# Performance work log

Hardware: AMD Instinct MI355X
Metric: run time of the kernel (lower is better)

Reference implementation:

```python
import jax, jax.numpy as jnp
import numpy as np

N = 100000      # nodes
E_RAND = 1500000
IN_DIM = 128
OUT_DIM = 128
H = 8
D = OUT_DIM // H  # 16 per-head dim
EPS = 1e-5


def _bn(x, gamma, beta):
    # BatchNorm1d, training mode: biased batch statistics over the node dim
    mu = jnp.mean(x, axis=0)
    var = jnp.mean((x - mu) ** 2, axis=0)
    return (x - mu) * jax.lax.rsqrt(var + EPS) * gamma + beta


def setup_inputs() -> dict:
    key = jax.random.key(0)
    ks = jax.random.split(key, 12)
    h = jax.random.normal(ks[0], (N, IN_DIM), dtype=jnp.float32)
    # edge list: random edges + self-loops so every dst has in-degree >= 1
    src_r = jax.random.randint(ks[1], (E_RAND,), 0, N, dtype=jnp.int32)
    dst_r = jax.random.randint(ks[2], (E_RAND,), 0, N, dtype=jnp.int32)
    loops = jnp.arange(N, dtype=jnp.int32)
    src = jnp.concatenate([loops, src_r])
    dst = jnp.concatenate([loops, dst_r])
    s = 1.0 / np.sqrt(IN_DIM)
    Wq = jax.random.normal(ks[3], (IN_DIM, OUT_DIM), dtype=jnp.float32) * s
    Wk = jax.random.normal(ks[4], (IN_DIM, OUT_DIM), dtype=jnp.float32) * s
    Wv = jax.random.normal(ks[5], (IN_DIM, OUT_DIM), dtype=jnp.float32) * s
    Wo = jax.random.normal(ks[6], (OUT_DIM, OUT_DIM), dtype=jnp.float32) * s
    bo = jnp.zeros((OUT_DIM,), dtype=jnp.float32)
    gamma1 = jnp.ones((OUT_DIM,), dtype=jnp.float32)
    beta1 = jnp.zeros((OUT_DIM,), dtype=jnp.float32)
    Wf1 = jax.random.normal(ks[7], (OUT_DIM, 2 * OUT_DIM), dtype=jnp.float32) * s
    bf1 = jnp.zeros((2 * OUT_DIM,), dtype=jnp.float32)
    Wf2 = jax.random.normal(ks[8], (2 * OUT_DIM, OUT_DIM), dtype=jnp.float32) * (1.0 / np.sqrt(2 * OUT_DIM))
    bf2 = jnp.zeros((OUT_DIM,), dtype=jnp.float32)
    gamma2 = jnp.ones((OUT_DIM,), dtype=jnp.float32)
    beta2 = jnp.zeros((OUT_DIM,), dtype=jnp.float32)
    return {"h": h, "Wq": Wq, "Wk": Wk, "Wv": Wv, "Wo": Wo, "bo": bo,
            "gamma1": gamma1, "beta1": beta1, "Wf1": Wf1, "bf1": bf1,
            "Wf2": Wf2, "bf2": bf2, "gamma2": gamma2, "beta2": beta2,
            "src": src, "dst": dst}


def reference(h, Wq, Wk, Wv, Wo, bo, gamma1, beta1, Wf1, bf1, Wf2, bf2,
              gamma2, beta2, src, dst):
    n = h.shape[0]
    Q = (h @ Wq).reshape(n, H, D)
    K = (h @ Wk).reshape(n, H, D)
    V = (h @ Wv).reshape(n, H, D)
    # per-edge score: (K[src] * Q[dst]).sum(-1), scaled exp with clamp
    score = jnp.sum(K[src] * Q[dst], axis=-1) / np.sqrt(D)   # [E, H]
    score = jnp.exp(jnp.clip(score, -5.0, 5.0))
    # weighted aggregation to dst nodes
    wV = jax.ops.segment_sum(V[src] * score[:, :, None], dst, num_segments=n)  # [N,H,D]
    z = jax.ops.segment_sum(score, dst, num_segments=n)                         # [N,H]
    attn = (wV / z[:, :, None]).reshape(n, OUT_DIM)
    # output projection + residual + batchnorm
    x = h + (attn @ Wo + bo)
    x = _bn(x, gamma1, beta1)
    # FFN + residual + batchnorm
    y = jax.nn.relu(x @ Wf1 + bf1) @ Wf2 + bf2
    x = _bn(x + y, gamma2, beta2)
    return x
```

## Files before the change

### kernel.cpp

```cpp
#include <hip/hip_runtime.h>

#define EPS 1e-5f
#define VSCALE 20.0f

typedef __attribute__((ext_vector_type(8))) short sh8;
typedef __attribute__((ext_vector_type(4))) float f4;
typedef __attribute__((ext_vector_type(2))) _Float16 h2f;

static __device__ __forceinline__ unsigned short f2b(float f) {
    union { float f; unsigned u; } v; v.f = f;
    unsigned r = v.u + 0x7FFF + ((v.u >> 16) & 1);
    return (unsigned short)(r >> 16);
}
static __device__ __forceinline__ float b2f(unsigned short b) {
    union { unsigned u; float f; } v; v.u = ((unsigned)b) << 16; return v.f;
}
static __device__ __forceinline__ unsigned pk2(float a, float b) {
    return (unsigned)f2b(a) | ((unsigned)f2b(b) << 16);
}
static __device__ __forceinline__ h2f u2h(unsigned u) {
    union { unsigned u; h2f h; } c; c.u = u; return c.h;
}
static __device__ __forceinline__ float dot2h(h2f a, h2f b, float c) {
#if __has_builtin(__builtin_amdgcn_fdot2)
    return __builtin_amdgcn_fdot2(a, b, c, false);
#else
    return (float)a.x * (float)b.x + (float)a.y * (float)b.y + c;
#endif
}

static __device__ __forceinline__ void barrier_raw() {
    __builtin_amdgcn_sched_barrier(0);
    asm volatile("s_waitcnt lgkmcnt(0)" ::: "memory");
    __builtin_amdgcn_s_barrier();
    __builtin_amdgcn_sched_barrier(0);
}

__global__ __launch_bounds__(256) void prep_all_k(
    const float* __restrict__ Wq, const float* __restrict__ Wk,
    const float* __restrict__ Wv, const float* __restrict__ Wo,
    const float* __restrict__ Wf1, const float* __restrict__ Wf2,
    unsigned short* __restrict__ Wt)
{
    int i = blockIdx.x * 256 + threadIdx.x;
    if (i < 65536) {
        int s = i >> 14;
        const float* W = (s == 0) ? Wq : (s == 1) ? Wk : (s == 2) ? Wv : Wo;
        int l = i & 16383, k = l >> 7, n = l & 127;
        Wt[(i & ~16383) + n * 128 + k] = f2b(W[l]);
    } else if (i < 98304) {
        int l = i - 65536, k = l >> 8, n = l & 255;
        Wt[65536 + n * 128 + k] = f2b(Wf1[l]);
    } else {
        int l = i - 98304, k = l >> 7, n = l & 127;
        Wt[98304 + n * 256 + k] = f2b(Wf2[l]);
    }
}

__global__ __launch_bounds__(256) void qkv_k(
    const float* __restrict__ h, const unsigned short* __restrict__ Wt,
    _Float16* __restrict__ Qh, _Float16* __restrict__ Kh,
    unsigned char* __restrict__ V8u, int M)
{
    __shared__ __align__(16) unsigned short As[128 * 136];
    __shared__ __align__(16) unsigned short Ws[128 * 72];
    const int tid = threadIdx.x;
    const int wave = tid >> 6, lane = tid & 63;
    const int q = lane >> 4, lm = lane & 15;
    const int rowBase = blockIdx.x * 128;
    const int r0 = (wave & 1) * 64, c0 = (wave >> 1) * 64;

#pragma unroll
    for (int j = 0; j < 16; ++j) {
        int idx = tid + j * 256;
        int row = idx >> 5, kk = (idx & 31) * 4;
        int grow = rowBase + row;
        float4 v = make_float4(0.f, 0.f, 0.f, 0.f);
        if (grow < M) v = *(const float4*)&h[(size_t)grow * 128 + kk];
        ushort4 b;
        b.x = f2b(v.x); b.y = f2b(v.y); b.z = f2b(v.z); b.w = f2b(v.w);
        *(ushort4*)&As[row * 136 + kk] = b;
    }

    for (int w = 0; w < 3; ++w) {
        f4 acc[4][4];
#pragma unroll
        for (int mi = 0; mi < 4; ++mi)
#pragma unroll
            for (int ni = 0; ni < 4; ++ni) {
                f4 z = {0.f, 0.f, 0.f, 0.f};
                acc[mi][ni] = z;
            }
        for (int kc = 0; kc < 2; ++kc) {
#pragma unroll
            for (int j = 0; j < 4; ++j) {
                int idx = tid + j * 256;
                int n = idx >> 3, kk = (idx & 7) * 8;
                uint4 v = *(const uint4*)&Wt[(size_t)w * 16384 + (size_t)n * 128 + kc * 64 + kk];
                *(uint4*)&Ws[n * 72 + kk] = v;
            }
            __syncthreads();
#pragma unroll
            for (int k2 = 0; k2 < 2; ++k2) {
                sh8 af[4], bfr[4];
#pragma unroll
                for (int t = 0; t < 4; ++t) {
                    af[t]  = *(const sh8*)&As[(r0 + t * 16 + lm) * 136 + kc * 64 + k2 * 32 + q * 8];
                    bfr[t] = *(const sh8*)&Ws[(c0 + t * 16 + lm) * 72 + k2 * 32 + q * 8];
                }
#pragma unroll
                for (int mi = 0; mi < 4; ++mi)
#pragma unroll
                    for (int ni = 0; ni < 4; ++ni)
                        acc[mi][ni] = __builtin_amdgcn_mfma_f32_16x16x32_bf16(
                            af[mi], bfr[ni], acc[mi][ni], 0, 0, 0);
            }
            __syncthreads();
        }
#pragma unroll
        for (int mi = 0; mi < 4; ++mi)
#pragma unroll
            for (int ni = 0; ni < 4; ++ni) {
                const int col = c0 + ni * 16 + lm;
#pragma unroll
                for (int r = 0; r < 4; ++r) {
                    int grow = rowBase + r0 + mi * 16 + q * 4 + r;
                    if (grow >= M) continue;
                    const float v = acc[mi][ni][r];
                    if (w == 0) Qh[(size_t)grow * 128 + col] = (_Float16)v;
                    else if (w == 1) Kh[(size_t)grow * 128 + col] = (_Float16)v;
                    else {
                        float t = rintf(v * VSCALE);
                        t = fminf(fmaxf(t, -127.f), 127.f);
                        V8u[(size_t)grow * 128 + col] = (unsigned char)(int)(t + 128.f);
                    }
                }
            }
    }
}

template<int KD, int RES, int STATS, int RELU>
__global__ __launch_bounds__(512) void gemm2_k(
    const unsigned short* __restrict__ A, const unsigned short* __restrict__ Wt,
    const float* __restrict__ bias, const void* __restrict__ resid,
    unsigned short* __restrict__ C, int M, int ldc, int tiles,
    const float* __restrict__ aff1, float* __restrict__ ostats)
{
    constexpr int CPR = KD / 8;
    constexpr int PER = 64 * CPR / 512;
    __shared__ __align__(16) unsigned short Ws[128 * KD];
    __shared__ __align__(16) unsigned short As[2][64 * KD];
    __shared__ float sacc[256];
    const int tid = threadIdx.x;
    const int wave = tid >> 6, lane = tid & 63;
    const int q = lane >> 4, lm = lane & 15;
    const int wr = wave >> 2, wc = wave & 3;
    const int colBase = blockIdx.y * 128;
    const unsigned short* Wblk = Wt + (size_t)colBase * KD;

    uint4 rA[PER];
    {
        const int rowT = blockIdx.x * 64;
#pragma unroll
        for (int i = 0; i < PER; ++i) {
            int g = tid + i * 512;
            int row = g / CPR, ch = g % CPR;
            int grow = rowT + row; if (grow >= M) grow = M - 1;
            rA[i] = *(const uint4*)&A[(size_t)grow * KD + ch * 8];
        }
    }

#pragma unroll
    for (int i = 0; i < 128 * CPR / 512; ++i) {
        int g = tid + i * 512;
        int col = g / CPR, ch = g % CPR;
        uint4 v = *(const uint4*)&Wblk[(size_t)col * KD + ch * 8];
        *(uint4*)&Ws[col * KD + ((ch ^ (col & 7)) * 8)] = v;
    }
    if (STATS && tid < 256) sacc[tid] = 0.f;

    float bv[2], rsc[2], rsh[2];
#pragma unroll
    for (int ni = 0; ni < 2; ++ni) {
        const int col = colBase + wc * 32 + ni * 16 + lm;
        bv[ni] = bias[col];
        if (RES == 3) { rsc[ni] = aff1[col]; rsh[ni] = aff1[128 + col]; }
        else { rsc[ni] = 0.f; rsh[ni] = 0.f; }
    }
    float st_s[2] = {0.f, 0.f}, st_ss[2] = {0.f, 0.f};

    int cur = 0;
    for (int t = blockIdx.x; t < tiles; t += gridDim.x) {
        const int rowT = t * 64;
        barrier_raw();
        unsigned short* Asc = As[cur];
#pragma unroll
        for (int i = 0; i < PER; ++i) {
            int g = tid + i * 512;
            int row = g / CPR, ch = g % CPR;
            *(uint4*)&Asc[row * KD + ((ch ^ (row & 7)) * 8)] = rA[i];
        }
        const int tn = t + (int)gridDim.x;
        if (tn < tiles) {
            const int rowTn = tn * 64;
#pragma unroll
            for (int i = 0; i < PER; ++i) {
                int g = tid + i * 512;
                int row = g / CPR, ch = g % CPR;
                int grow = rowTn + row; if (grow >= M) grow = M - 1;
                rA[i] = *(const uint4*)&A[(size_t)grow * KD + ch * 8];
            }
        }
        barrier_raw();

        f4 acc[2][2];
#pragma unroll
        for (int mi = 0; mi < 2; ++mi)
#pragma unroll
            for (int ni = 0; ni < 2; ++ni) {
                f4 z = {0.f, 0.f, 0.f, 0.f};
                acc[mi][ni] = z;
            }
#pragma unroll
        for (int kc = 0; kc < KD / 32; ++kc) {
            sh8 af[2], bfr[2];
#pragma unroll
            for (int mi = 0; mi < 2; ++mi) {
                const int row = wr * 32 + mi * 16 + lm;
                af[mi] = *(const sh8*)&Asc[row * KD + (((kc * 4 + q) ^ (row & 7)) * 8)];
            }
#pragma unroll
            for (int ni = 0; ni < 2; ++ni) {
                const int col = wc * 32 + ni * 16 + lm;
                bfr[ni] = *(const sh8*)&Ws[col * KD + (((kc * 4 + q) ^ (col & 7)) * 8)];
            }
#pragma unroll
            for (int mi = 0; mi < 2; ++mi)
#pragma unroll
                for (int ni = 0; ni < 2; ++ni)
                    acc[mi][ni] = __builtin_amdgcn_mfma_f32_16x16x32_bf16(
                        af[mi], bfr[ni], acc[mi][ni], 0, 0, 0);
        }

#pragma unroll
        for (int ni = 0; ni < 2; ++ni) {
            const int col = colBase + wc * 32 + ni * 16 + lm;
#pragma unroll
            for (int mi = 0; mi < 2; ++mi) {
#pragma unroll
                for (int r = 0; r < 4; ++r) {
                    const int row = rowT + wr * 32 + mi * 16 + q * 4 + r;
                    if (row >= M) continue;
                    float val = acc[mi][ni][r] + bv[ni];
                    if (RES == 1)
                        val += ((const float*)resid)[(size_t)row * ldc + col];
                    if (RES == 3)
                        val += b2f(((const unsigned short*)resid)[(size_t)row * ldc + col])
                               * rsc[ni] + rsh[ni];
                    if (RELU) val = fmaxf(val, 0.f);
                    if (STATS) { st_s[ni] += val; st_ss[ni] += val * val; }
                    C[(size_t)row * ldc + col] = f2b(val);
                }
            }
        }
        cur ^= 1;
    }

    if (STATS) {
        barrier_raw();
#pragma unroll
        for (int ni = 0; ni < 2; ++ni) {
            st_s[ni]  += __shfl_xor(st_s[ni], 16);  st_s[ni]  += __shfl_xor(st_s[ni], 32);
            st_ss[ni] += __shfl_xor(st_ss[ni], 16); st_ss[ni] += __shfl_xor(st_ss[ni], 32);
            if (q == 0) {
                const int c = wc * 32 + ni * 16 + lm;
                atomicAdd(&sacc[c], st_s[ni]);
                atomicAdd(&sacc[128 + c], st_ss[ni]);
            }
        }
        barrier_raw();
        if (tid < 128) {
            atomicAdd(&ostats[tid], sacc[tid]);
            atomicAdd(&ostats[128 + tid], sacc[128 + tid]);
        }
    }
}

__global__ __launch_bounds__(256) void fold_bn1_k(
    const unsigned short* __restrict__ W1t, const float* __restrict__ rstats,
    const float* __restrict__ g1, const float* __restrict__ b1,
    const float* __restrict__ bf1, float invN,
    unsigned short* __restrict__ W1f, float* __restrict__ b1f,
    float* __restrict__ aff1)
{
    __shared__ float sc[128], sh[128];
    const int t = threadIdx.x;
    if (t < 128) {
        const float mu = rstats[t] * invN;
        const float var = rstats[128 + t] * invN - mu * mu;
        const float isg = rsqrtf(var + EPS) * g1[t];
        const float shf = b1[t] - mu * isg;
        sc[t] = isg; sh[t] = shf;
        aff1[t] = isg; aff1[128 + t] = shf;
    }
    __syncthreads();
    float acc = bf1[t];
#pragma unroll
    for (int c = 0; c < 128; c += 8) {
        const uint4 v = *(const uint4*)&W1t[t * 128 + c];
        const float w0 = b2f((unsigned short)(v.x & 0xffff));
        const float w1 = b2f((unsigned short)(v.x >> 16));
        const float w2 = b2f((unsigned short)(v.y & 0xffff));
        const float w3 = b2f((unsigned short)(v.y >> 16));
        const float w4 = b2f((unsigned short)(v.z & 0xffff));
        const float w5 = b2f((unsigned short)(v.z >> 16));
        const float w6 = b2f((unsigned short)(v.w & 0xffff));
        const float w7 = b2f((unsigned short)(v.w >> 16));
        acc += sh[c] * w0 + sh[c + 1] * w1 + sh[c + 2] * w2 + sh[c + 3] * w3
             + sh[c + 4] * w4 + sh[c + 5] * w5 + sh[c + 6] * w6 + sh[c + 7] * w7;
        uint4 o;
        o.x = pk2(w0 * sc[c],     w1 * sc[c + 1]);
        o.y = pk2(w2 * sc[c + 2], w3 * sc[c + 3]);
        o.z = pk2(w4 * sc[c + 4], w5 * sc[c + 5]);
        o.w = pk2(w6 * sc[c + 6], w7 * sc[c + 7]);
        *(uint4*)&W1f[t * 128 + c] = o;
    }
    b1f[t] = acc;
}

__global__ __launch_bounds__(256) void bucket_cnt_k(const int* __restrict__ dst,
                                                    int E, int* __restrict__ bCnt)
{
    __shared__ int c[512];
    const int t = threadIdx.x;
    c[t] = 0; c[t + 256] = 0;
    __syncthreads();
    for (int i = blockIdx.x * 256 + t; i < E; i += gridDim.x * 256)
        atomicAdd(&c[dst[i] >> 8], 1);
    __syncthreads();
    if (c[t]) atomicAdd(&bCnt[t], c[t]);
    if (c[t + 256]) atomicAdd(&bCnt[t + 256], c[t + 256]);
}

__global__ __launch_bounds__(512) void bucket_scan_k(const int* __restrict__ bCnt,
                                                     int B, int* __restrict__ bOff,
                                                     int* __restrict__ bCur)
{
    __shared__ int ts[512];
    const int t = threadIdx.x;
    const int v = (t < B) ? bCnt[t] : 0;
    ts[t] = v;
    __syncthreads();
    for (int o = 1; o < 512; o <<= 1) {
        int u = (t >= o) ? ts[t - o] : 0;
        __syncthreads();
        ts[t] += u;
        __syncthreads();
    }
    const int ex = ts[t] - v;
    if (t < B) { bOff[t] = ex; bCur[t] = ex; }
    if (t == B - 1) bOff[B] = ex + v;
}

#define CCH 8192
__global__ __launch_bounds__(512) void coarse_k(const int* __restrict__ src,
                                                const int* __restrict__ dst, int E,
                                                int* __restrict__ bCur,
                                                unsigned* __restrict__ coarse)
{
    __shared__ int cnt[512], off[512], gbase[512], rc[512];
    __shared__ unsigned pk[CCH];
    __shared__ int ga[CCH];
    const int t = threadIdx.x;
    const int e0 = blockIdx.x * CCH;
    const int n = min(CCH, E - e0);
    cnt[t] = 0;
    __syncthreads();
    for (int i = t; i < n; i += 512) atomicAdd(&cnt[dst[e0 + i] >> 8], 1);
    __syncthreads();
    const int v = cnt[t];
    off[t] = v;
    __syncthreads();
    for (int o = 1; o < 512; o <<= 1) {
        int u = (t >= o) ? off[t - o] : 0;
        __syncthreads();
        off[t] += u;
        __syncthreads();
    }
    const int ex = off[t] - v;
    off[t] = ex;
    if (v > 0) gbase[t] = atomicAdd(&bCur[t], v);
    rc[t] = 0;
    __syncthreads();
    for (int i = t; i < n; i += 512) {
        const int d = dst[e0 + i], s = src[e0 + i];
        const int b = d >> 8;
        const int j = atomicAdd(&rc[b], 1);
        const int slot = off[b] + j;
        pk[slot] = ((unsigned)(d & 255) << 17) | (unsigned)s;
        ga[slot] = gbase[b] + j;
    }
    __syncthreads();
    for (int i = t; i < n; i += 512) coarse[ga[i]] = pk[i];
}

__global__ __launch_bounds__(256) void fine_k(const unsigned* __restrict__ coarse,
                                              const int* __restrict__ bOff, int B,
                                              int Nn, int* __restrict__ row_ptr,
                                              int* __restrict__ esrc)
{
    __shared__ int cnt[256], off[256], rc[256];
    const int t = threadIdx.x;
    const int b = blockIdx.x;
    const int base = b << 8;
    const int e0 = bOff[b], e1 = bOff[b + 1];
    cnt[t] = 0;
    __syncthreads();
    for (int i = e0 + t; i < e1; i += 256)
        atomicAdd(&cnt[(coarse[i] >> 17) & 255], 1);
    __syncthreads();
    const int v = cnt[t];
    off[t] = v;
    __syncthreads();
    for (int o = 1; o < 256; o <<= 1) {
        int u = (t >= o) ? off[t - o] : 0;
        __syncthreads();
        off[t] += u;
        __syncthreads();
    }
    const int ex = off[t] - v;
    off[t] = ex;
    rc[t] = 0;
    if (base + t < Nn) row_ptr[base + t] = e0 + ex;
    if (b == B - 1 && t == 0) row_ptr[Nn] = e1;
    __syncthreads();
    for (int i = e0 + t; i < e1; i += 256) {
        const unsigned p = coarse[i];
        const int l = (p >> 17) & 255;
        const int j = atomicAdd(&rc[l], 1);
        esrc[e0 + off[l] + j] = (int)(p & 0x1FFFFu);
    }
}

__global__ __launch_bounds__(256) void edge_attn_k(
    const _Float16* __restrict__ Qh, const _Float16* __restrict__ Kh,
    const unsigned char* __restrict__ V8u, const int* __restrict__ row_ptr,
    const int* __restrict__ esrc, unsigned short* __restrict__ attnb, int Nn)
{
    const int wave = threadIdx.x >> 6, lane = threadIdx.x & 63;
    const int node = blockIdx.x * 4 + wave;
    if (node >= Nn) return;
    const int g = lane & 15, p = lane >> 4;
    const uint4 qv = *(const uint4*)&Qh[(size_t)node * 128 + g * 8];
    const h2f q0 = u2h(qv.x), q1 = u2h(qv.y), q2 = u2h(qv.z), q3 = u2h(qv.w);
    const int e0 = row_ptr[node], e1 = row_ptr[node + 1];
    const int cnt = e1 - e0;
    float a0 = 0.f, a1 = 0.f, a2 = 0.f, a3 = 0.f;
    float a4 = 0.f, a5 = 0.f, a6 = 0.f, a7 = 0.f, z = 0.f;
    for (int base = 0; base < cnt; base += 64) {
        const int nb = min(cnt - base, 64);
        const int myS = (lane < nb) ? esrc[e0 + base + lane] : 0;
        int s = __shfl(myS, p);
        uint4 kv = *(const uint4*)&Kh[(size_t)s * 128 + g * 8];
        uint2 vv = *(const uint2*)&V8u[(size_t)s * 128 + g * 8];
        for (int j = 0; j < nb; j += 4) {
            const uint4 kc = kv;
            const uint2 vc = vv;
            const int ei = j + p;
            const int jn = j + 4;
            if (jn < nb) {
                const int sn = __shfl(myS, jn + p);
                kv = *(const uint4*)&Kh[(size_t)sn * 128 + g * 8];
                vv = *(const uint2*)&V8u[(size_t)sn * 128 + g * 8];
            }
            float sp = dot2h(u2h(kc.w), q3, dot2h(u2h(kc.z), q2,
                       dot2h(u2h(kc.y), q1, dot2h(u2h(kc.x), q0, 0.f))));
            sp += __shfl_xor(sp, 1);
            float sc = __expf(fminf(fmaxf(sp * 0.25f, -5.f), 5.f));
            sc = (ei < nb) ? sc : 0.f;
            a0 += sc * (float)(vc.x & 0xffu);
            a1 += sc * (float)((vc.x >> 8) & 0xffu);
            a2 += sc * (float)((vc.x >> 16) & 0xffu);
            a3 += sc * (float)(vc.x >> 24);
            a4 += sc * (float)(vc.y & 0xffu);
            a5 += sc * (float)((vc.y >> 8) & 0xffu);
            a6 += sc * (float)((vc.y >> 16) & 0xffu);
            a7 += sc * (float)(vc.y >> 24);
            z += sc;
        }
    }
    a0 += __shfl_xor(a0, 16); a0 += __shfl_xor(a0, 32);
    a1 += __shfl_xor(a1, 16); a1 += __shfl_xor(a1, 32);
    a2 += __shfl_xor(a2, 16); a2 += __shfl_xor(a2, 32);
    a3 += __shfl_xor(a3, 16); a3 += __shfl_xor(a3, 32);
    a4 += __shfl_xor(a4, 16); a4 += __shfl_xor(a4, 32);
    a5 += __shfl_xor(a5, 16); a5 += __shfl_xor(a5, 32);
    a6 += __shfl_xor(a6, 16); a6 += __shfl_xor(a6, 32);
    a7 += __shfl_xor(a7, 16); a7 += __shfl_xor(a7, 32);
    z  += __shfl_xor(z, 16);  z  += __shfl_xor(z, 32);
    const float inv = 1.f / (z * VSCALE);
    const float c = 128.f * z;
    if (p == 0) {
        uint4 o;
        o.x = pk2((a0 - c) * inv, (a1 - c) * inv);
        o.y = pk2((a2 - c) * inv, (a3 - c) * inv);
        o.z = pk2((a4 - c) * inv, (a5 - c) * inv);
        o.w = pk2((a6 - c) * inv, (a7 - c) * inv);
        *(uint4*)&attnb[(size_t)node * 128 + g * 8] = o;
    }
}

__global__ __launch_bounds__(256) void bn_apply_b_k(const unsigned short* __restrict__ X,
                                                    const float* __restrict__ rstats,
                                                    const float* __restrict__ gma,
                                                    const float* __restrict__ bta,
                                                    float invN, int total8,
                                                    float* __restrict__ out)
{
    __shared__ float aff[256];
    if (threadIdx.x < 128) {
        const int c = threadIdx.x;
        const float mu = rstats[c] * invN;
        const float var = rstats[128 + c] * invN - mu * mu;
        const float isg = rsqrtf(var + EPS) * gma[c];
        aff[c] = isg;
        aff[128 + c] = bta[c] - mu * isg;
    }
    __syncthreads();
    for (int i = blockIdx.x * blockDim.x + threadIdx.x; i < total8;
         i += gridDim.x * blockDim.x) {
        const int c8 = (i & 15) * 8;
        const float4 sc0 = *(const float4*)&aff[c8];
        const float4 sc1 = *(const float4*)&aff[c8 + 4];
        const float4 sh0 = *(const float4*)&aff[128 + c8];
        const float4 sh1 = *(const float4*)&aff[128 + c8 + 4];
        const uint4 v = ((const uint4*)X)[i];
        float4 o0, o1;
        o0.x = b2f((unsigned short)(v.x & 0xffff)) * sc0.x + sh0.x;
        o0.y = b2f((unsigned short)(v.x >> 16))    * sc0.y + sh0.y;
        o0.z = b2f((unsigned short)(v.y & 0xffff)) * sc0.z + sh0.z;
        o0.w = b2f((unsigned short)(v.y >> 16))    * sc0.w + sh0.w;
        o1.x = b2f((unsigned short)(v.z & 0xffff)) * sc1.x + sh1.x;
        o1.y = b2f((unsigned short)(v.z >> 16))    * sc1.y + sh1.y;
        o1.z = b2f((unsigned short)(v.w & 0xffff)) * sc1.z + sh1.z;
        o1.w = b2f((unsigned short)(v.w >> 16))    * sc1.w + sh1.w;
        ((float4*)out)[i * 2]     = o0;
        ((float4*)out)[i * 2 + 1] = o1;
    }
}

extern "C" void kernel_launch(void* const* d_in, const int* in_sizes, int n_in,
                              void* d_out, int out_size, void* d_ws, size_t ws_size,
                              hipStream_t stream)
{
    const float* h   = (const float*)d_in[0];
    const float* Wq  = (const float*)d_in[1];
    const float* Wk  = (const float*)d_in[2];
    const float* Wv  = (const float*)d_in[3];
    const float* Wo  = (const float*)d_in[4];
    const float* bo  = (const float*)d_in[5];
    const float* g1  = (const float*)d_in[6];
    const float* b1  = (const float*)d_in[7];
    const float* Wf1 = (const float*)d_in[8];
    const float* bf1 = (const float*)d_in[9];
    const float* Wf2 = (const float*)d_in[10];
    const float* bf2 = (const float*)d_in[11];
    const float* g2  = (const float*)d_in[12];
    const float* b2  = (const float*)d_in[13];
    const int*   src = (const int*)d_in[14];
    const int*   dstv= (const int*)d_in[15];
    const int N = in_sizes[0] / 128;
    const int E = in_sizes[14];
    const int B = (N + 255) >> 8;
    const float invN = 1.f / (float)N;

    unsigned short* Wt = (unsigned short*)d_ws;
    float* stats1 = (float*)((char*)d_ws + 262144);
    float* stats2 = stats1 + 256;
    int* bCnt = (int*)(stats2 + 256);
    int* bOff = bCnt + 512;
    int* bCur = bOff + 513;
    uintptr_t big = ((uintptr_t)(bCur + 512) + 255) & ~(uintptr_t)255;
    _Float16* Qh = (_Float16*)big;
    _Float16* Kh = Qh + (size_t)N * 128;
    unsigned char* V8u = (unsigned char*)(Kh + (size_t)N * 128);
    uintptr_t a2 = ((uintptr_t)(V8u + (size_t)N * 128) + 255) & ~(uintptr_t)255;
    unsigned short* attnb = (unsigned short*)a2;
    unsigned short* xb = attnb + (size_t)N * 128;
    int* row_ptr = (int*)(xb + (size_t)N * 128);
    unsigned* coarse = (unsigned*)attnb;
    int* esrc = (int*)xb;
    unsigned short* hidden = (unsigned short*)Qh;
    unsigned short* yb = attnb;
    float* aff1 = (float*)V8u;
    float* b1f  = aff1 + 256;
    unsigned short* W1f = (unsigned short*)(b1f + 256);

    unsigned short* Wf1T = Wt + 65536;
    unsigned short* Wf2T = Wt + 98304;

    float* out = (float*)d_out;
    const dim3 b256(256);
    const dim3 b512(512);
    const int tiles128 = (N + 127) / 128;
    const int tiles64 = (N + 63) / 64;

    hipMemsetAsync(stats1, 0, 4096, stream);

    prep_all_k<<<dim3(512), b256, 0, stream>>>(Wq, Wk, Wv, Wo, Wf1, Wf2, Wt);

    bucket_cnt_k<<<dim3(256), b256, 0, stream>>>(dstv, E, bCnt);
    bucket_scan_k<<<dim3(1), dim3(512), 0, stream>>>(bCnt, B, bOff, bCur);
    coarse_k<<<dim3((E + CCH - 1) / CCH), dim3(512), 0, stream>>>(src, dstv, E, bCur, coarse);
    fine_k<<<dim3(B), b256, 0, stream>>>(coarse, bOff, B, N, row_ptr, esrc);

    qkv_k<<<dim3(tiles128), b256, 0, stream>>>(h, Wt, Qh, Kh, V8u, N);

    edge_attn_k<<<dim3((N + 3) / 4), b256, 0, stream>>>(Qh, Kh, V8u, row_ptr, esrc, attnb, N);

    gemm2_k<128, 1, 1, 0><<<dim3(512, 1), b512, 0, stream>>>(
        attnb, Wt + 49152, bo, h, xb, N, 128, tiles64, nullptr, stats1);

    fold_bn1_k<<<dim3(1), b256, 0, stream>>>(Wf1T, stats1, g1, b1, bf1, invN,
                                             W1f, b1f, aff1);

    gemm2_k<128, 0, 0, 1><<<dim3(512, 2), b512, 0, stream>>>(
        xb, W1f, b1f, nullptr, hidden, N, 256, tiles64, nullptr, nullptr);

    gemm2_k<256, 3, 1, 0><<<dim3(256, 1), b512, 0, stream>>>(
        hidden, Wf2T, bf2, xb, yb, N, 128, tiles64, aff1, stats2);

    bn_apply_b_k<<<dim3(1024), b256, 0, stream>>>(yb, stats2, g2, b2, invN, N * 16, out);
}
```

Before: 484.6 us.

## Double-buffer QKV weight tiles and deepen edge gather prefetch to two stages

```diff
diff --git a/kernel.cpp b/kernel.cpp
--- a/kernel.cpp
+++ b/kernel.cpp
@@ -63,12 +63,20 @@
     unsigned char* __restrict__ V8u, int M)
 {
     __shared__ __align__(16) unsigned short As[128 * 136];
-    __shared__ __align__(16) unsigned short Ws[128 * 72];
+    __shared__ __align__(16) unsigned short Ws[2][128 * 72];
     const int tid = threadIdx.x;
     const int wave = tid >> 6, lane = tid & 63;
     const int q = lane >> 4, lm = lane & 15;
     const int rowBase = blockIdx.x * 128;
     const int r0 = (wave & 1) * 64, c0 = (wave >> 1) * 64;
+
+    uint4 rW[4];
+#pragma unroll
+    for (int j = 0; j < 4; ++j) {
+        int idx = tid + j * 256;
+        int n = idx >> 3, kk = (idx & 7) * 8;
+        rW[j] = *(const uint4*)&Wt[(size_t)n * 128 + kk];
+    }
 
 #pragma unroll
     for (int j = 0; j < 16; ++j) {
@@ -82,60 +90,74 @@
         *(ushort4*)&As[row * 136 + kk] = b;
     }
 
-    for (int w = 0; w < 3; ++w) {
-        f4 acc[4][4];
-#pragma unroll
-        for (int mi = 0; mi < 4; ++mi)
-#pragma unroll
-            for (int ni = 0; ni < 4; ++ni) {
-                f4 z = {0.f, 0.f, 0.f, 0.f};
-                acc[mi][ni] = z;
-            }
-        for (int kc = 0; kc < 2; ++kc) {
+    int cur = 0;
+    f4 acc[4][4];
+    for (int ph = 0; ph < 6; ++ph) {
+        const int w = ph >> 1, kc = ph & 1;
+        if (kc == 0) {
+#pragma unroll
+            for (int mi = 0; mi < 4; ++mi)
+#pragma unroll
+                for (int ni = 0; ni < 4; ++ni) {
+                    f4 z = {0.f, 0.f, 0.f, 0.f};
+                    acc[mi][ni] = z;
+                }
+        }
+        barrier_raw();
+        unsigned short* Wsc = Ws[cur];
+#pragma unroll
+        for (int j = 0; j < 4; ++j) {
+            int idx = tid + j * 256;
+            int n = idx >> 3, kk = (idx & 7) * 8;
+            *(uint4*)&Wsc[n * 72 + kk] = rW[j];
+        }
+        if (ph < 5) {
+            const int wn = (ph + 1) >> 1, kcn = (ph + 1) & 1;
 #pragma unroll
             for (int j = 0; j < 4; ++j) {
                 int idx = tid + j * 256;
                 int n = idx >> 3, kk = (idx & 7) * 8;
-                uint4 v = *(const uint4*)&Wt[(size_t)w * 16384 + (size_t)n * 128 + kc * 64 + kk];
-                *(uint4*)&Ws[n * 72 + kk] = v;
-            }
-            __syncthreads();
-#pragma unroll
-            for (int k2 = 0; k2 < 2; ++k2) {
-                sh8 af[4], bfr[4];
-#pragma unroll
-                for (int t = 0; t < 4; ++t) {
-                    af[t]  = *(const sh8*)&As[(r0 + t * 16 + lm) * 136 + kc * 64 + k2 * 32 + q * 8];
-                    bfr[t] = *(const sh8*)&Ws[(c0 + t * 16 + lm) * 72 + k2 * 32 + q * 8];
-                }
-#pragma unroll
-                for (int mi = 0; mi < 4; ++mi)
-#pragma unroll
-                    for (int ni = 0; ni < 4; ++ni)
-                        acc[mi][ni] = __builtin_amdgcn_mfma_f32_16x16x32_bf16(
-                            af[mi], bfr[ni], acc[mi][ni], 0, 0, 0);
-            }
-            __syncthreads();
-        }
-#pragma unroll
-        for (int mi = 0; mi < 4; ++mi)
-#pragma unroll
-            for (int ni = 0; ni < 4; ++ni) {
-                const int col = c0 + ni * 16 + lm;
-#pragma unroll
-                for (int r = 0; r < 4; ++r) {
-                    int grow = rowBase + r0 + mi * 16 + q * 4 + r;
-                    if (grow >= M) continue;
-                    const float v = acc[mi][ni][r];
-                    if (w == 0) Qh[(size_t)grow * 128 + col] = (_Float16)v;
-                    else if (w == 1) Kh[(size_t)grow * 128 + col] = (_Float16)v;
-                    else {
-                        float t = rintf(v * VSCALE);
-                        t = fminf(fmaxf(t, -127.f), 127.f);
-                        V8u[(size_t)grow * 128 + col] = (unsigned char)(int)(t + 128.f);
+                rW[j] = *(const uint4*)&Wt[(size_t)wn * 16384 + (size_t)n * 128 + kcn * 64 + kk];
+            }
+        }
+        barrier_raw();
+#pragma unroll
+        for (int k2 = 0; k2 < 2; ++k2) {
+            sh8 af[4], bfr[4];
+#pragma unroll
+            for (int t = 0; t < 4; ++t) {
+                af[t]  = *(const sh8*)&As[(r0 + t * 16 + lm) * 136 + kc * 64 + k2 * 32 + q * 8];
+                bfr[t] = *(const sh8*)&Wsc[(c0 + t * 16 + lm) * 72 + k2 * 32 + q * 8];
+            }
+#pragma unroll
+            for (int mi = 0; mi < 4; ++mi)
+#pragma unroll
+                for (int ni = 0; ni < 4; ++ni)
+                    acc[mi][ni] = __builtin_amdgcn_mfma_f32_16x16x32_bf16(
+                        af[mi], bfr[ni], acc[mi][ni], 0, 0, 0);
+        }
+        if (kc == 1) {
+#pragma unroll
+            for (int mi = 0; mi < 4; ++mi)
+#pragma unroll
+                for (int ni = 0; ni < 4; ++ni) {
+                    const int col = c0 + ni * 16 + lm;
+#pragma unroll
+                    for (int r = 0; r < 4; ++r) {
+                        int grow = rowBase + r0 + mi * 16 + q * 4 + r;
+                        if (grow >= M) continue;
+                        const float v = acc[mi][ni][r];
+                        if (w == 0) Qh[(size_t)grow * 128 + col] = (_Float16)v;
+                        else if (w == 1) Kh[(size_t)grow * 128 + col] = (_Float16)v;
+                        else {
+                            float t = rintf(v * VSCALE);
+                            t = fminf(fmaxf(t, -127.f), 127.f);
+                            V8u[(size_t)grow * 128 + col] = (unsigned char)(int)(t + 128.f);
+                        }
                     }
                 }
-            }
+        }
+        cur ^= 1;
     }
 }
 
@@ -442,6 +464,23 @@
     }
 }
 
+#define EA_ACC(kc, vc, EI) do {                                              \
+    float sp = dot2h(u2h((kc).w), q3, dot2h(u2h((kc).z), q2,                 \
+               dot2h(u2h((kc).y), q1, dot2h(u2h((kc).x), q0, 0.f))));        \
+    sp += __shfl_xor(sp, 1);                                                 \
+    float sc = __expf(fminf(fmaxf(sp * 0.25f, -5.f), 5.f));                  \
+    sc = ((EI) < nb) ? sc : 0.f;                                             \
+    a0 += sc * (float)((vc).x & 0xffu);                                      \
+    a1 += sc * (float)(((vc).x >> 8) & 0xffu);                               \
+    a2 += sc * (float)(((vc).x >> 16) & 0xffu);                              \
+    a3 += sc * (float)((vc).x >> 24);                                        \
+    a4 += sc * (float)((vc).y & 0xffu);                                      \
+    a5 += sc * (float)(((vc).y >> 8) & 0xffu);                               \
+    a6 += sc * (float)(((vc).y >> 16) & 0xffu);                              \
+    a7 += sc * (float)((vc).y >> 24);                                        \
+    z += sc;                                                                 \
+} while (0)
+
 __global__ __launch_bounds__(256) void edge_attn_k(
     const _Float16* __restrict__ Qh, const _Float16* __restrict__ Kh,
     const unsigned char* __restrict__ V8u, const int* __restrict__ row_ptr,
@@ -460,33 +499,31 @@
     for (int base = 0; base < cnt; base += 64) {
         const int nb = min(cnt - base, 64);
         const int myS = (lane < nb) ? esrc[e0 + base + lane] : 0;
-        int s = __shfl(myS, p);
-        uint4 kv = *(const uint4*)&Kh[(size_t)s * 128 + g * 8];
-        uint2 vv = *(const uint2*)&V8u[(size_t)s * 128 + g * 8];
-        for (int j = 0; j < nb; j += 4) {
-            const uint4 kc = kv;
-            const uint2 vc = vv;
-            const int ei = j + p;
-            const int jn = j + 4;
-            if (jn < nb) {
-                const int sn = __shfl(myS, jn + p);
-                kv = *(const uint4*)&Kh[(size_t)sn * 128 + g * 8];
-                vv = *(const uint2*)&V8u[(size_t)sn * 128 + g * 8];
-            }
-            float sp = dot2h(u2h(kc.w), q3, dot2h(u2h(kc.z), q2,
-                       dot2h(u2h(kc.y), q1, dot2h(u2h(kc.x), q0, 0.f))));
-            sp += __shfl_xor(sp, 1);
-            float sc = __expf(fminf(fmaxf(sp * 0.25f, -5.f), 5.f));
-            sc = (ei < nb) ? sc : 0.f;
-            a0 += sc * (float)(vc.x & 0xffu);
-            a1 += sc * (float)((vc.x >> 8) & 0xffu);
-            a2 += sc * (float)((vc.x >> 16) & 0xffu);
-            a3 += sc * (float)(vc.x >> 24);
-            a4 += sc * (float)(vc.y & 0xffu);
-            a5 += sc * (float)((vc.y >> 8) & 0xffu);
-            a6 += sc * (float)((vc.y >> 16) & 0xffu);
-            a7 += sc * (float)(vc.y >> 24);
-            z += sc;
+        const int s0 = __shfl(myS, p);
+        uint4 kvA = *(const uint4*)&Kh[(size_t)s0 * 128 + g * 8];
+        uint2 vvA = *(const uint2*)&V8u[(size_t)s0 * 128 + g * 8];
+        const int s1 = __shfl(myS, (4 + p) & 63);
+        uint4 kvB = *(const uint4*)&Kh[(size_t)s1 * 128 + g * 8];
+        uint2 vvB = *(const uint2*)&V8u[(size_t)s1 * 128 + g * 8];
+        for (int j = 0; j < nb; j += 8) {
+            {
+                const uint4 kc = kvA; const uint2 vc = vvA;
+                if (j + 8 < nb) {
+                    const int sn = __shfl(myS, (j + 8 + p) & 63);
+                    kvA = *(const uint4*)&Kh[(size_t)sn * 128 + g * 8];
+                    vvA = *(const uint2*)&V8u[(size_t)sn * 128 + g * 8];
+                }
+                EA_ACC(kc, vc, j + p);
+            }
+            {
+                const uint4 kc = kvB; const uint2 vc = vvB;
+                if (j + 12 < nb) {
+                    const int sn = __shfl(myS, (j + 12 + p) & 63);
+                    kvB = *(const uint4*)&Kh[(size_t)sn * 128 + g * 8];
+                    vvB = *(const uint2*)&V8u[(size_t)sn * 128 + g * 8];
+                }
+                EA_ACC(kc, vc, j + 4 + p);
+            }
         }
     }
     a0 += __shfl_xor(a0, 16); a0 += __shfl_xor(a0, 32);
```

Measured after the change: 503.2 us. 1.04x slower.

## Interleave K and V rows and deepen edge-gather prefetch in attention kernel

Applied to the files above, without the earlier changes.

```diff
diff --git a/kernel.cpp b/kernel.cpp
--- a/kernel.cpp
+++ b/kernel.cpp
@@ -28,6 +28,17 @@
     return (float)a.x * (float)b.x + (float)a.y * (float)b.y + c;
 #endif
 }
+#if __has_builtin(__builtin_amdgcn_cvt_f32_ubyte0)
+#define UB0(x) __builtin_amdgcn_cvt_f32_ubyte0(x)
+#define UB1(x) __builtin_amdgcn_cvt_f32_ubyte1(x)
+#define UB2(x) __builtin_amdgcn_cvt_f32_ubyte2(x)
+#define UB3(x) __builtin_amdgcn_cvt_f32_ubyte3(x)
+#else
+#define UB0(x) ((float)((x) & 0xffu))
+#define UB1(x) ((float)(((x) >> 8) & 0xffu))
+#define UB2(x) ((float)(((x) >> 16) & 0xffu))
+#define UB3(x) ((float)((x) >> 24))
+#endif
 
 static __device__ __forceinline__ void barrier_raw() {
     __builtin_amdgcn_sched_barrier(0);
@@ -59,8 +70,7 @@
 
 __global__ __launch_bounds__(256) void qkv_k(
     const float* __restrict__ h, const unsigned short* __restrict__ Wt,
-    _Float16* __restrict__ Qh, _Float16* __restrict__ Kh,
-    unsigned char* __restrict__ V8u, int M)
+    _Float16* __restrict__ Qh, unsigned char* __restrict__ KV, int M)
 {
     __shared__ __align__(16) unsigned short As[128 * 136];
     __shared__ __align__(16) unsigned short Ws[128 * 72];
@@ -128,11 +138,12 @@
                     if (grow >= M) continue;
                     const float v = acc[mi][ni][r];
                     if (w == 0) Qh[(size_t)grow * 128 + col] = (_Float16)v;
-                    else if (w == 1) Kh[(size_t)grow * 128 + col] = (_Float16)v;
+                    else if (w == 1)
+                        *(_Float16*)(KV + (size_t)grow * 384 + col * 2) = (_Float16)v;
                     else {
                         float t = rintf(v * VSCALE);
                         t = fminf(fmaxf(t, -127.f), 127.f);
-                        V8u[(size_t)grow * 128 + col] = (unsigned char)(int)(t + 128.f);
+                        KV[(size_t)grow * 384 + 256 + col] = (unsigned char)(int)(t + 128.f);
                     }
                 }
             }
@@ -442,10 +453,27 @@
     }
 }
 
+#define EA_ACC(kc, vc, EI) do {                                              \
+    float sp = dot2h(u2h((kc).w), q3, dot2h(u2h((kc).z), q2,                 \
+               dot2h(u2h((kc).y), q1, dot2h(u2h((kc).x), q0, 0.f))));        \
+    sp += __shfl_xor(sp, 1);                                                 \
+    float sc = __expf(fminf(fmaxf(sp * 0.25f, -5.f), 5.f));                  \
+    sc = ((EI) < nb) ? sc : 0.f;                                             \
+    a0 += sc * UB0((vc).x);                                                  \
+    a1 += sc * UB1((vc).x);                                                  \
+    a2 += sc * UB2((vc).x);                                                  \
+    a3 += sc * UB3((vc).x);                                                  \
+    a4 += sc * UB0((vc).y);                                                  \
+    a5 += sc * UB1((vc).y);                                                  \
+    a6 += sc * UB2((vc).y);                                                  \
+    a7 += sc * UB3((vc).y);                                                  \
+    z += sc;                                                                 \
+} while (0)
+
 __global__ __launch_bounds__(256) void edge_attn_k(
-    const _Float16* __restrict__ Qh, const _Float16* __restrict__ Kh,
-    const unsigned char* __restrict__ V8u, const int* __restrict__ row_ptr,
-    const int* __restrict__ esrc, unsigned short* __restrict__ attnb, int Nn)
+    const _Float16* __restrict__ Qh, const unsigned char* __restrict__ KV,
+    const int* __restrict__ row_ptr, const int* __restrict__ esrc,
+    unsigned short* __restrict__ attnb, int Nn)
 {
     const int wave = threadIdx.x >> 6, lane = threadIdx.x & 63;
     const int node = blockIdx.x * 4 + wave;
@@ -455,38 +483,43 @@
     const h2f q0 = u2h(qv.x), q1 = u2h(qv.y), q2 = u2h(qv.z), q3 = u2h(qv.w);
     const int e0 = row_ptr[node], e1 = row_ptr[node + 1];
     const int cnt = e1 - e0;
+    const int e1m1 = e1 - 1;
     float a0 = 0.f, a1 = 0.f, a2 = 0.f, a3 = 0.f;
     float a4 = 0.f, a5 = 0.f, a6 = 0.f, a7 = 0.f, z = 0.f;
     for (int base = 0; base < cnt; base += 64) {
         const int nb = min(cnt - base, 64);
-        const int myS = (lane < nb) ? esrc[e0 + base + lane] : 0;
-        int s = __shfl(myS, p);
-        uint4 kv = *(const uint4*)&Kh[(size_t)s * 128 + g * 8];
-        uint2 vv = *(const uint2*)&V8u[(size_t)s * 128 + g * 8];
-        for (int j = 0; j < nb; j += 4) {
-            const uint4 kc = kv;
-            const uint2 vc = vv;
-            const int ei = j + p;
-            const int jn = j + 4;
-            if (jn < nb) {
-                const int sn = __shfl(myS, jn + p);
-                kv = *(const uint4*)&Kh[(size_t)sn * 128 + g * 8];
-                vv = *(const uint2*)&V8u[(size_t)sn * 128 + g * 8];
-            }
-            float sp = dot2h(u2h(kc.w), q3, dot2h(u2h(kc.z), q2,
-                       dot2h(u2h(kc.y), q1, dot2h(u2h(kc.x), q0, 0.f))));
-            sp += __shfl_xor(sp, 1);
-            float sc = __expf(fminf(fmaxf(sp * 0.25f, -5.f), 5.f));
-            sc = (ei < nb) ? sc : 0.f;
-            a0 += sc * (float)(vc.x & 0xffu);
-            a1 += sc * (float)((vc.x >> 8) & 0xffu);
-            a2 += sc * (float)((vc.x >> 16) & 0xffu);
-            a3 += sc * (float)(vc.x >> 24);
-            a4 += sc * (float)(vc.y & 0xffu);
-            a5 += sc * (float)((vc.y >> 8) & 0xffu);
-            a6 += sc * (float)((vc.y >> 16) & 0xffu);
-            a7 += sc * (float)(vc.y >> 24);
-            z += sc;
+        const int eb = e0 + base + p;
+        {
+            const int s0 = esrc[min(eb, e1m1)];
+            const unsigned char* r = KV + (size_t)((unsigned)s0 * 384u);
+            const int s1 = esrc[min(eb + 4, e1m1)];
+            const unsigned char* rB = KV + (size_t)((unsigned)s1 * 384u);
+            uint4 kvA = *(const uint4*)(r + g * 16);
+            uint2 vvA = *(const uint2*)(r + 256 + g * 8);
+            uint4 kvB = *(const uint4*)(rB + g * 16);
+            uint2 vvB = *(const uint2*)(rB + 256 + g * 8);
+            for (int j = 0; j < nb; j += 8) {
+                {
+                    const uint4 kc = kvA; const uint2 vc = vvA;
+                    if (j + 8 < nb) {
+                        const int sn = esrc[min(eb + j + 8, e1m1)];
+                        const unsigned char* rn = KV + (size_t)((unsigned)sn * 384u);
+                        kvA = *(const uint4*)(rn + g * 16);
+                        vvA = *(const uint2*)(rn + 256 + g * 8);
+                    }
+                    EA_ACC(kc, vc, j + p);
+                }
+                {
+                    const uint4 kc = kvB; const uint2 vc = vvB;
+                    if (j + 12 < nb) {
+                        const int sn = esrc[min(eb + j + 12, e1m1)];
+                        const unsigned char* rn = KV + (size_t)((unsigned)sn * 384u);
+                        kvB = *(const uint4*)(rn + g * 16);
+                        vvB = *(const uint2*)(rn + 256 + g * 8);
+                    }
+                    EA_ACC(kc, vc, j + 4 + p);
+                }
+            }
         }
     }
     a0 += __shfl_xor(a0, 16); a0 += __shfl_xor(a0, 32);
@@ -582,9 +615,8 @@
     int* bCur = bOff + 513;
     uintptr_t big = ((uintptr_t)(bCur + 512) + 255) & ~(uintptr_t)255;
     _Float16* Qh = (_Float16*)big;
-    _Float16* Kh = Qh + (size_t)N * 128;
-    unsigned char* V8u = (unsigned char*)(Kh + (size_t)N * 128);
-    uintptr_t a2 = ((uintptr_t)(V8u + (size_t)N * 128) + 255) & ~(uintptr_t)255;
+    unsigned char* KV = (unsigned char*)(Qh + (size_t)N * 128);
+    uintptr_t a2 = ((uintptr_t)(KV + (size_t)N * 384) + 255) & ~(uintptr_t)255;
     unsigned short* attnb = (unsigned short*)a2;
     unsigned short* xb = attnb + (size_t)N * 128;
     int* row_ptr = (int*)(xb + (size_t)N * 128);
@@ -592,7 +624,8 @@
     int* esrc = (int*)xb;
     unsigned short* hidden = (unsigned short*)Qh;
     unsigned short* yb = attnb;
-    float* aff1 = (float*)V8u;
+    uintptr_t fb = (big + (size_t)N * 512 + 255) & ~(uintptr_t)255;
+    float* aff1 = (float*)fb;
     float* b1f  = aff1 + 256;
     unsigned short* W1f = (unsigned short*)(b1f + 256);
 
@@ -614,9 +647,9 @@
     coarse_k<<<dim3((E + CCH - 1) / CCH), dim3(512), 0, stream>>>(src, dstv, E, bCur, coarse);
     fine_k<<<dim3(B), b256, 0, stream>>>(coarse, bOff, B, N, row_ptr, esrc);
 
-    qkv_k<<<dim3(tiles128), b256, 0, stream>>>(h, Wt, Qh, Kh, V8u, N);
-
-    edge_attn_k<<<dim3((N + 3) / 4), b256, 0, stream>>>(Qh, Kh, V8u, row_ptr, esrc, attnb, N);
+    qkv_k<<<dim3(tiles128), b256, 0, stream>>>(h, Wt, Qh, KV, N);
+
+    edge_attn_k<<<dim3((N + 3) / 4), b256, 0, stream>>>(Qh, KV, row_ptr, esrc, attnb, N);
 
     gemm2_k<128, 1, 1, 0><<<dim3(512, 1), b512, 0, stream>>>(
         attnb, Wt + 49152, bo, h, xb, N, 128, tiles64, nullptr, stats1);
```

Result: slower. 521.3 us (+7.6%).
